# Kernel tuning notes

Measured on AMD Instinct MI355X. Metric: run time of the kernel, lower is better.

The kernel has to match this reference:

```python
import jax, jax.numpy as jnp
import numpy as np

EMBED_DIM = 1024
NUM_HEADS = 16
HEAD_DIM = EMBED_DIM // NUM_HEADS


def setup_inputs() -> dict:
    key = jax.random.key(0)
    k1, k2, k3 = jax.random.split(key, 3)
    B, S = 4, 2048
    scale = 1.0 / np.sqrt(EMBED_DIM)
    x = jax.random.normal(k1, (B, S, EMBED_DIM), dtype=jnp.float32)
    w_qkv = jax.random.normal(k2, (EMBED_DIM, 3 * EMBED_DIM), dtype=jnp.float32) * scale
    b_qkv = jnp.zeros((3 * EMBED_DIM,), dtype=jnp.float32)
    w_proj = jax.random.normal(k3, (EMBED_DIM, EMBED_DIM), dtype=jnp.float32) * scale
    b_proj = jnp.zeros((EMBED_DIM,), dtype=jnp.float32)
    return {"x": x, "w_qkv": w_qkv, "b_qkv": b_qkv, "w_proj": w_proj, "b_proj": b_proj}


def reference(x, w_qkv, b_qkv, w_proj, b_proj):
    # x: [B, S, E]. Dropout is identity in eval mode.
    B, S, E = x.shape
    qkv = x @ w_qkv + b_qkv                                  # [B, S, 3E]
    qkv = qkv.reshape(B, S, 3, NUM_HEADS, HEAD_DIM)
    qkv = jnp.transpose(qkv, (2, 0, 3, 1, 4))                # [3, B, H, S, Dh]
    q, k, v = qkv[0], qkv[1], qkv[2]
    scores = jnp.einsum("bhsd,bhtd->bhst", q, k) / np.sqrt(HEAD_DIM)
    probs = jax.nn.softmax(scores, axis=-1)                  # [B, H, S, S]
    out = jnp.einsum("bhst,bhtd->bhsd", probs, v)            # [B, H, S, Dh]
    out = jnp.transpose(out, (0, 2, 1, 3)).reshape(B, S, E)
    return out @ w_proj + b_proj
```

## Files before the change

### kernel.cpp

```cpp
#include <hip/hip_runtime.h>

typedef unsigned short u16;
typedef __bf16 bf16x8_v __attribute__((ext_vector_type(8)));
typedef unsigned short u16x8 __attribute__((ext_vector_type(8)));
typedef unsigned short u16x4 __attribute__((ext_vector_type(4)));
typedef unsigned short u16x2 __attribute__((ext_vector_type(2)));
typedef float f32x4 __attribute__((ext_vector_type(4)));

typedef const __attribute__((address_space(1))) void* gas_ptr;
typedef __attribute__((address_space(3))) void* las_ptr;

static __device__ __forceinline__ u16 f2bf(float f) {
  unsigned int u = __builtin_bit_cast(unsigned int, f);
  u = (u + 0x7fffu + ((u >> 16) & 1u)) >> 16;
  return (u16)u;
}

static __device__ __forceinline__ f32x4 mfma16(u16x8 a, u16x8 b, f32x4 c) {
  return __builtin_amdgcn_mfma_f32_16x16x32_bf16(
      __builtin_bit_cast(bf16x8_v, a), __builtin_bit_cast(bf16x8_v, b), c, 0, 0, 0);
}

static __device__ __forceinline__ f32x4 mfma16v(bf16x8_v a, bf16x8_v b, f32x4 c) {
  return __builtin_amdgcn_mfma_f32_16x16x32_bf16(a, b, c, 0, 0, 0);
}

static __device__ __forceinline__ void gload_lds16(const u16* g, u16* lds) {
  __builtin_amdgcn_global_load_lds((gas_ptr)g, (las_ptr)lds, 16, 0, 0);
}

__global__ __launch_bounds__(256) void cvt_bf16(const float* __restrict__ in,
                                                u16* __restrict__ out, int n4) {
  int i = blockIdx.x * 256 + threadIdx.x;
  if (i >= n4) return;
  float4 v = ((const float4*)in)[i];
  ushort4 o;
  o.x = f2bf(v.x); o.y = f2bf(v.y); o.z = f2bf(v.z); o.w = f2bf(v.w);
  ((ushort4*)out)[i] = o;
}

__global__ __launch_bounds__(256) void transpose_cvt(const float* __restrict__ w,
                                                     u16* __restrict__ wt, int K, int N) {
  __shared__ float t[32][33];
  const int n0 = blockIdx.x * 32, k0 = blockIdx.y * 32;
  const int tx = threadIdx.x & 31, ty = threadIdx.x >> 5;
#pragma unroll
  for (int i = 0; i < 4; ++i) {
    int k = ty + i * 8;
    t[k][tx] = w[(size_t)(k0 + k) * N + n0 + tx];
  }
  __syncthreads();
#pragma unroll
  for (int i = 0; i < 4; ++i) {
    int n = ty + i * 8;
    wt[(size_t)(n0 + n) * K + k0 + tx] = f2bf(t[tx][n]);
  }
}

template <bool BF16_OUT>
__global__ __launch_bounds__(256)
void gemm_bt(const u16* __restrict__ A, const u16* __restrict__ Bt,
             const float* __restrict__ bias, void* __restrict__ Cv,
             int M, int N, int K) {
  __shared__ u16 As[128 * 32];
  __shared__ u16 Bs[128 * 32];
  const int tid = threadIdx.x;
  const int l = tid & 63, w = tid >> 6;
  const int lr = l & 15, lg = l >> 4;
  const int wr = w >> 1, wc = w & 1;
  const int nx = gridDim.x, nwg = nx * gridDim.y;
  int id = blockIdx.y * nx + blockIdx.x;
  id = (id & 7) * (nwg >> 3) + (id >> 3);
  const int m0 = (id / nx) * 128, n0 = (id % nx) * 128;

  f32x4 acc[4][4];
#pragma unroll
  for (int i = 0; i < 4; ++i)
#pragma unroll
    for (int j = 0; j < 4; ++j) acc[i][j] = f32x4{0.f, 0.f, 0.f, 0.f};

  for (int ks = 0; ks < K; ks += 32) {
#pragma unroll
    for (int i = 0; i < 2; ++i) {
      const int c = i * 256 + w * 64 + l;
      const int row = c >> 2, kc = (c & 3) << 3;
      gload_lds16(A + (size_t)(m0 + row) * K + ks + kc, &As[(i * 256 + w * 64) * 8]);
      gload_lds16(Bt + (size_t)(n0 + row) * K + ks + kc, &Bs[(i * 256 + w * 64) * 8]);
    }
    __syncthreads();
    u16x8 af[4], bfr[4];
#pragma unroll
    for (int m = 0; m < 4; ++m)
      af[m] = *(const u16x8*)&As[(wr * 64 + m * 16 + lr) * 32 + lg * 8];
#pragma unroll
    for (int n = 0; n < 4; ++n)
      bfr[n] = *(const u16x8*)&Bs[(wc * 64 + n * 16 + lr) * 32 + lg * 8];
#pragma unroll
    for (int m = 0; m < 4; ++m)
#pragma unroll
      for (int n = 0; n < 4; ++n)
        acc[m][n] = mfma16(af[m], bfr[n], acc[m][n]);
    __syncthreads();
  }

#pragma unroll
  for (int m = 0; m < 4; ++m) {
    const int grow = m0 + wr * 64 + m * 16 + lg * 4;
#pragma unroll
    for (int n = 0; n < 4; ++n) {
      const int gcol = n0 + wc * 64 + n * 16 + lr;
      const float bv = bias[gcol];
#pragma unroll
      for (int r = 0; r < 4; ++r) {
        const float v = acc[m][n][r] + bv;
        if (BF16_OUT)
          ((u16*)Cv)[(size_t)(grow + r) * N + gcol] = f2bf(v);
        else
          ((float*)Cv)[(size_t)(grow + r) * N + gcol] = v;
      }
    }
  }
}

__global__ __launch_bounds__(256)
void attn64(const u16* __restrict__ qkv, u16* __restrict__ ctx, int bhmask, int bhbits) {
  constexpr int S = 2048, E3 = 3072, E = 1024;
  __shared__ u16 Ks[2][64 * 64];
  __shared__ u16 Vt[64 * 64];
  char* VtB = (char*)Vt;
  const int tid = threadIdx.x, l = tid & 63, w = tid >> 6;
  const int lr = l & 15, lg = l >> 4;
  const int p = blockIdx.x;
  const int bh = p & bhmask, qt = p >> bhbits;
  const int b = bh >> 4, h = bh & 15;
  const u16* base = qkv + (size_t)b * S * E3;
  const int qcol = h * 64, kcol = E + h * 64, vcol = 2 * E + h * 64;
  const int s0 = qt * 64;
  const float C2 = 0.1803368801f;

  bf16x8_v onesv;
  {
    u16x8 ou;
#pragma unroll
    for (int e = 0; e < 8; ++e) ou[e] = (lr == 0) ? (u16)0x3F80 : (u16)0;
    onesv = __builtin_bit_cast(bf16x8_v, ou);
  }

  u16x8 qf[2];
  {
    const u16* qp = base + (size_t)(s0 + w * 16 + lr) * E3 + qcol + lg * 8;
    u16x8 q0 = *(const u16x8*)qp;
    u16x8 q1 = *(const u16x8*)(qp + 32);
#pragma unroll
    for (int e = 0; e < 8; ++e) {
      float a0 = (float)__builtin_bit_cast(bf16x8_v, q0)[e] * C2;
      float a1 = (float)__builtin_bit_cast(bf16x8_v, q1)[e] * C2;
      qf[0][e] = __builtin_bit_cast(u16, (__bf16)a0);
      qf[1][e] = __builtin_bit_cast(u16, (__bf16)a1);
    }
  }

  f32x4 o[4];
#pragma unroll
  for (int d = 0; d < 4; ++d) o[d] = f32x4{0.f, 0.f, 0.f, 0.f};
  f32x4 ls = f32x4{0.f, 0.f, 0.f, 0.f};

  const int tp = tid >> 3, d0v = (tid & 7) << 3;
  const u16* vp0 = base + vcol + d0v + (size_t)(tp * 2) * E3;

  u16x8 va = *(const u16x8*)vp0;
  u16x8 vb8 = *(const u16x8*)(vp0 + E3);
#pragma unroll
  for (int i = 0; i < 2; ++i) {
    const int c = i * 256 + tid;
    const int t = c >> 3;
    const int sc = ((c & 7) ^ (t & 7)) << 3;
    gload_lds16(base + (size_t)t * E3 + kcol + sc, &Ks[0][(i * 256 + w * 64) * 8]);
  }

  for (int kt = 0; kt < S; kt += 64) {
    const int cur = (kt >> 6) & 1;
    __builtin_amdgcn_s_barrier();
#pragma unroll
    for (int e = 0; e < 8; ++e) {
      const int row = d0v + e;
      u16x2 pr;
      pr[0] = va[e];
      pr[1] = vb8[e];
      *(u16x2*)&VtB[row * 128 + ((tp * 4) ^ ((row & 15) << 3))] = pr;
    }
    const int ktn = (kt + 64 < S) ? kt + 64 : 0;
    {
      const u16* vpn = vp0 + (size_t)ktn * E3;
      va = *(const u16x8*)vpn;
      vb8 = *(const u16x8*)(vpn + E3);
#pragma unroll
      for (int i = 0; i < 2; ++i) {
        const int c = i * 256 + tid;
        const int t = c >> 3;
        const int sc = ((c & 7) ^ (t & 7)) << 3;
        gload_lds16(base + (size_t)(ktn + t) * E3 + kcol + sc,
                    &Ks[cur ^ 1][(i * 256 + w * 64) * 8]);
      }
    }
    asm volatile("s_waitcnt vmcnt(4) lgkmcnt(0)" ::: "memory");
    __builtin_amdgcn_sched_barrier(0);
    __builtin_amdgcn_s_barrier();

    char* KsB = (char*)Ks[cur];
    f32x4 sacc[4];
#pragma unroll
    for (int tf = 0; tf < 4; ++tf) sacc[tf] = f32x4{0.f, 0.f, 0.f, 0.f};
#pragma unroll
    for (int kk = 0; kk < 2; ++kk)
#pragma unroll
      for (int tf = 0; tf < 4; ++tf) {
        const int row = tf * 16 + lr;
        u16x8 kf = *(const u16x8*)&KsB[row * 128 + ((kk * 64 + lg * 16) ^ ((row & 7) << 4))];
        sacc[tf] = mfma16(kf, qf[kk], sacc[tf]);
      }

#pragma unroll
    for (int tf = 0; tf < 4; ++tf)
#pragma unroll
      for (int r = 0; r < 4; ++r)
        sacc[tf][r] = exp2f(sacc[tf][r]);

#pragma unroll
    for (int kk = 0; kk < 2; ++kk) {
      bf16x8_v pav;
#pragma unroll
      for (int e = 0; e < 8; ++e) pav[e] = (__bf16)sacc[2 * kk + (e >> 2)][e & 3];
#pragma unroll
      for (int dt = 0; dt < 4; ++dt) {
        const int row = dt * 16 + lr;
        const int cb = kk * 64 + lg * 8;
        const int sw = (row & 15) << 3;
        u16x4 vlo = *(const u16x4*)&VtB[row * 128 + (cb ^ sw)];
        u16x4 vhi = *(const u16x4*)&VtB[row * 128 + ((cb + 32) ^ sw)];
        bf16x8_v vf = __builtin_bit_cast(bf16x8_v,
            __builtin_shufflevector(vlo, vhi, 0, 1, 2, 3, 4, 5, 6, 7));
        o[dt] = mfma16v(pav, vf, o[dt]);
      }
      ls = mfma16v(pav, onesv, ls);
    }
  }

#pragma unroll
  for (int r = 0; r < 4; ++r) {
    const float den = __shfl(ls[r], l & 48, 64);
    const float ir = 1.0f / den;
    const int row = s0 + w * 16 + 4 * lg + r;
    const size_t rb = ((size_t)b * S + row) * E + h * 64;
#pragma unroll
    for (int dt = 0; dt < 4; ++dt)
      ctx[rb + dt * 16 + lr] = __builtin_bit_cast(u16, (__bf16)(o[dt][r] * ir));
  }
}

extern "C" void kernel_launch(void* const* d_in, const int* in_sizes, int n_in,
                              void* d_out, int out_size, void* d_ws, size_t ws_size,
                              hipStream_t stream) {
  const float* x = (const float*)d_in[0];
  const float* w_qkv = (const float*)d_in[1];
  const float* b_qkv = (const float*)d_in[2];
  const float* w_proj = (const float*)d_in[3];
  const float* b_proj = (const float*)d_in[4];
  float* out = (float*)d_out;

  const int B = 4, S = 2048, E = 1024;

  const size_t E2 = (size_t)E * E, SE = (size_t)S * E;
  int NB = 1;
  if (ws_size >= 2 * (4 * E2 + 16 * SE)) NB = 4;
  else if (ws_size >= 2 * (4 * E2 + 8 * SE)) NB = 2;

  u16* ws = (u16*)d_ws;
  u16* wqkvt = ws;
  u16* wprojt = wqkvt + 3 * E2;
  u16* xbf   = wprojt + E2;
  u16* qkvb  = xbf + (size_t)NB * SE;
  u16* ctx   = xbf;

  transpose_cvt<<<dim3(3 * E / 32, E / 32), 256, 0, stream>>>(w_qkv, wqkvt, E, 3 * E);
  transpose_cvt<<<dim3(E / 32, E / 32), 256, 0, stream>>>(w_proj, wprojt, E, E);

  const int nbh = NB * 16;
  int bhbits = 4;
  if (NB == 2) bhbits = 5;
  if (NB == 4) bhbits = 6;

  for (int g = 0; g < B; g += NB) {
    const int Mg = NB * S;
    const float* xg = x + (size_t)g * SE;
    float* outg = out + (size_t)g * SE;
    cvt_bf16<<<(Mg * E / 4 + 255) / 256, 256, 0, stream>>>(xg, xbf, Mg * E / 4);
    gemm_bt<true><<<dim3(3 * E / 128, Mg / 128), 256, 0, stream>>>(xbf, wqkvt, b_qkv, qkvb, Mg, 3 * E, E);
    attn64<<<dim3((S / 64) * nbh), 256, 0, stream>>>(qkvb, ctx, nbh - 1, bhbits);
    gemm_bt<false><<<dim3(E / 128, Mg / 128), 256, 0, stream>>>(ctx, wprojt, b_proj, outg, Mg, E, E);
  }
}
```

Baseline: 337.5 us.

## Double-buffer GEMM LDS tiles and re-swizzle V transpose buffer in attention

The bf16 GEMM now keeps two LDS buffers for A and B and prefetches the next K-slice with direct global-to-LDS loads while MFMAs run on the current one. This removes one of the two barriers per iteration and hides load latency, at the cost of twice the LDS use, which may lower occupancy. In the attention kernel the transposed-V XOR swizzle gains an extra per-16-row-block term to spread LDS bank accesses. The vmcnt wait threshold is raised from 4 to 6, presumably so the V register prefetch can stay in flight during the barrier.

Measured after the change: 310.7 us. 7.9% less time.

```diff
diff --git a/kernel.cpp b/kernel.cpp
--- a/kernel.cpp
+++ b/kernel.cpp
@@ -62,8 +62,8 @@
 void gemm_bt(const u16* __restrict__ A, const u16* __restrict__ Bt,
              const float* __restrict__ bias, void* __restrict__ Cv,
              int M, int N, int K) {
-  __shared__ u16 As[128 * 32];
-  __shared__ u16 Bs[128 * 32];
+  __shared__ u16 As[2][128 * 32];
+  __shared__ u16 Bs[2][128 * 32];
   const int tid = threadIdx.x;
   const int l = tid & 63, w = tid >> 6;
   const int lr = l & 15, lg = l >> 4;
@@ -79,28 +79,41 @@
 #pragma unroll
     for (int j = 0; j < 4; ++j) acc[i][j] = f32x4{0.f, 0.f, 0.f, 0.f};
 
+#pragma unroll
+  for (int i = 0; i < 2; ++i) {
+    const int c = i * 256 + w * 64 + l;
+    const int row = c >> 2, kc = (c & 3) << 3;
+    gload_lds16(A + (size_t)(m0 + row) * K + kc, &As[0][(i * 256 + w * 64) * 8]);
+    gload_lds16(Bt + (size_t)(n0 + row) * K + kc, &Bs[0][(i * 256 + w * 64) * 8]);
+  }
+
   for (int ks = 0; ks < K; ks += 32) {
+    const int cur = (ks >> 5) & 1;
+    __builtin_amdgcn_s_barrier();
+    const int ksn = (ks + 32 < K) ? ks + 32 : 0;
 #pragma unroll
     for (int i = 0; i < 2; ++i) {
       const int c = i * 256 + w * 64 + l;
       const int row = c >> 2, kc = (c & 3) << 3;
-      gload_lds16(A + (size_t)(m0 + row) * K + ks + kc, &As[(i * 256 + w * 64) * 8]);
-      gload_lds16(Bt + (size_t)(n0 + row) * K + ks + kc, &Bs[(i * 256 + w * 64) * 8]);
-    }
-    __syncthreads();
+      gload_lds16(A + (size_t)(m0 + row) * K + ksn + kc, &As[cur ^ 1][(i * 256 + w * 64) * 8]);
+      gload_lds16(Bt + (size_t)(n0 + row) * K + ksn + kc, &Bs[cur ^ 1][(i * 256 + w * 64) * 8]);
+    }
+    asm volatile("s_waitcnt vmcnt(4)" ::: "memory");
+    __builtin_amdgcn_sched_barrier(0);
+    __builtin_amdgcn_s_barrier();
+
     u16x8 af[4], bfr[4];
 #pragma unroll
     for (int m = 0; m < 4; ++m)
-      af[m] = *(const u16x8*)&As[(wr * 64 + m * 16 + lr) * 32 + lg * 8];
+      af[m] = *(const u16x8*)&As[cur][(wr * 64 + m * 16 + lr) * 32 + lg * 8];
 #pragma unroll
     for (int n = 0; n < 4; ++n)
-      bfr[n] = *(const u16x8*)&Bs[(wc * 64 + n * 16 + lr) * 32 + lg * 8];
+      bfr[n] = *(const u16x8*)&Bs[cur][(wc * 64 + n * 16 + lr) * 32 + lg * 8];
 #pragma unroll
     for (int m = 0; m < 4; ++m)
 #pragma unroll
       for (int n = 0; n < 4; ++n)
         acc[m][n] = mfma16(af[m], bfr[n], acc[m][n]);
-    __syncthreads();
   }
 
 #pragma unroll
@@ -184,10 +197,12 @@
 #pragma unroll
     for (int e = 0; e < 8; ++e) {
       const int row = d0v + e;
+      const int m = row >> 4;
+      const int g = ((m & 1) << 2) | (m & 2);
       u16x2 pr;
       pr[0] = va[e];
       pr[1] = vb8[e];
-      *(u16x2*)&VtB[row * 128 + ((tp * 4) ^ ((row & 15) << 3))] = pr;
+      *(u16x2*)&VtB[row * 128 + ((tp * 4) ^ (((row & 15) ^ g) << 3))] = pr;
     }
     const int ktn = (kt + 64 < S) ? kt + 64 : 0;
     {
@@ -203,7 +218,7 @@
                     &Ks[cur ^ 1][(i * 256 + w * 64) * 8]);
       }
     }
-    asm volatile("s_waitcnt vmcnt(4) lgkmcnt(0)" ::: "memory");
+    asm volatile("s_waitcnt vmcnt(6) lgkmcnt(0)" ::: "memory");
     __builtin_amdgcn_sched_barrier(0);
     __builtin_amdgcn_s_barrier();
 
@@ -234,8 +249,9 @@
 #pragma unroll
       for (int dt = 0; dt < 4; ++dt) {
         const int row = dt * 16 + lr;
+        const int g = ((dt & 1) << 2) | (dt & 2);
         const int cb = kk * 64 + lg * 8;
-        const int sw = (row & 15) << 3;
+        const int sw = ((lr ^ g) & 15) << 3;
         u16x4 vlo = *(const u16x4*)&VtB[row * 128 + (cb ^ sw)];
         u16x4 vhi = *(const u16x4*)&VtB[row * 128 + ((cb + 32) ^ sw)];
         bf16x8_v vf = __builtin_bit_cast(bf16x8_v,
```
